# Optimization experiments

Hardware: AMD Instinct MI355X
Metric: run time of the kernel (lower is better)

Reference implementation:

```python
import jax, jax.numpy as jnp
import numpy as np

D = 384
H = 6
DK = D // H
EPS = 1e-5


def _layernorm(x, g, b):
    mu = jnp.mean(x, axis=-1, keepdims=True)
    var = jnp.var(x, axis=-1, keepdims=True)
    return (x - mu) * jax.lax.rsqrt(var + EPS) * g + b


def setup_inputs() -> dict:
    key = jax.random.key(0)
    ks = jax.random.split(key, 12)
    B, N = 8, 2048
    s = lambda fan_in: 1.0 / np.sqrt(fan_in)
    return {
        "points": jax.random.normal(ks[0], (B, 3 + D, N), dtype=jnp.float32),
        "ln1_g": jnp.ones((D,), jnp.float32),
        "ln1_b": jnp.zeros((D,), jnp.float32),
        "w_qkv": jax.random.uniform(ks[1], (3 * D, D), jnp.float32, -s(D), s(D)),
        "w_o": jax.random.uniform(ks[2], (D, D), jnp.float32, -s(D), s(D)),
        "b_o": jnp.zeros((D,), jnp.float32),
        "ln2_g": jnp.ones((D,), jnp.float32),
        "ln2_b": jnp.zeros((D,), jnp.float32),
        "w1": jax.random.uniform(ks[3], (2 * D, D), jnp.float32, -s(D), s(D)),
        "b1": jnp.zeros((2 * D,), jnp.float32),
        "w2": jax.random.uniform(ks[4], (D, 2 * D), jnp.float32, -s(2 * D), s(2 * D)),
        "b2": jnp.zeros((D,), jnp.float32),
    }


def reference(points, ln1_g, ln1_b, w_qkv, w_o, b_o, ln2_g, ln2_b, w1, b1, w2, b2):
    coords = points[:, :3, :]                       # [B, 3, N]
    feats = jnp.transpose(points[:, 3:, :], (0, 2, 1))  # [B, N, D]
    B, N, _ = feats.shape

    # pre-norm + fused QKV projection (no bias)
    h = _layernorm(feats, ln1_g, ln1_b)
    qkv = jnp.einsum('bnd,ed->bne', h, w_qkv)       # [B, N, 3D]
    q, k, v = jnp.split(qkv, 3, axis=-1)

    split_heads = lambda t: jnp.transpose(t.reshape(B, N, H, DK), (0, 2, 1, 3))
    q, k, v = split_heads(q), split_heads(k), split_heads(v)  # [B, H, N, DK]

    scale = DK ** -0.5
    scores = jnp.einsum('bhid,bhjd->bhij', q, k) * scale      # [B, H, N, N]
    attn = jax.nn.softmax(scores, axis=-1)
    ctx = jnp.einsum('bhij,bhjd->bhid', attn, v)              # [B, H, N, DK]
    ctx = jnp.transpose(ctx, (0, 2, 1, 3)).reshape(B, N, D)
    attn_out = jnp.einsum('bnd,ed->bne', ctx, w_o) + b_o

    x = feats + attn_out
    # FFN with exact (erf) GELU, hidden = 2*D
    h2 = _layernorm(x, ln2_g, ln2_b)
    ff = jnp.einsum('bnd,ed->bne', h2, w1) + b1
    ff = jax.nn.gelu(ff, approximate=False)
    ff = jnp.einsum('bne,de->bnd', ff, w2) + b2
    x = x + ff

    return jnp.concatenate([coords, jnp.transpose(x, (0, 2, 1))], axis=1)
```

## Files before the change

kernel.cpp:

```cpp
#include <hip/hip_runtime.h>
#include <cstdint>


typedef __bf16 bf16;
typedef __bf16 bf16x8 __attribute__((ext_vector_type(8)));
typedef __bf16 bf16x4 __attribute__((ext_vector_type(4)));
typedef float floatx4 __attribute__((ext_vector_type(4)));
typedef uint32_t __attribute__((address_space(1))) gu32;
typedef uint32_t __attribute__((address_space(3))) lu32;

#define NN 2048
#define DD 384
#define HH 6
#define DK 64
#define BB 8
#define MM (BB * NN)
#define D3 (3 * DD)
#define D2 (2 * DD)
#define CH (3 + DD)
#define LP 72


__global__ void cast_w_kernel(const float* __restrict__ in, bf16* __restrict__ out, int n) {
    int i = blockIdx.x * 256 + threadIdx.x;
    if (i < n) out[i] = (bf16)in[i];
}

__global__ void coords_kernel(const float* __restrict__ pts, float* __restrict__ out) {
    int i = blockIdx.x * 256 + threadIdx.x;
    int b = i / (3 * NN), r = i % (3 * NN);
    out[(size_t)b * CH * NN + r] = pts[(size_t)b * CH * NN + r];
}

__global__ void transpose_kernel(const float* __restrict__ pts, float* __restrict__ feats) {
    __shared__ float T[32][33];
    int n0 = blockIdx.x * 32, d0 = blockIdx.y * 32, b = blockIdx.z;
    int tx = threadIdx.x, ty = threadIdx.y;
    const float* src = pts + (size_t)b * CH * NN;
#pragma unroll
    for (int i = 0; i < 4; ++i)
        T[ty + i * 8][tx] = src[(size_t)(3 + d0 + ty + i * 8) * NN + n0 + tx];
    __syncthreads();
    float* dst = feats + (size_t)b * NN * DD;
#pragma unroll
    for (int i = 0; i < 4; ++i)
        dst[(size_t)(n0 + ty + i * 8) * DD + d0 + tx] = T[tx][ty + i * 8];
}

__global__ __launch_bounds__(256) void ln_kernel(const float* __restrict__ x,
                                                 const float* __restrict__ g,
                                                 const float* __restrict__ bta,
                                                 bf16* __restrict__ out) {
    int wave = threadIdx.x >> 6, lane = threadIdx.x & 63;
    int row = blockIdx.x * 4 + wave;
    const float* xr = x + (size_t)row * DD;
    float v[6], s = 0.f, sq = 0.f;
#pragma unroll
    for (int i = 0; i < 6; ++i) { v[i] = xr[lane + i * 64]; s += v[i]; sq += v[i] * v[i]; }
#pragma unroll
    for (int o = 1; o < 64; o <<= 1) { s += __shfl_xor(s, o); sq += __shfl_xor(sq, o); }
    float mu = s * (1.f / DD);
    float var = sq * (1.f / DD) - mu * mu;
    float rs = rsqrtf(var + 1e-5f);
    bf16* orow = out + (size_t)row * DD;
#pragma unroll
    for (int i = 0; i < 6; ++i) {
        int d = lane + i * 64;
        orow[d] = (bf16)((v[i] - mu) * rs * g[d] + bta[d]);
    }
}

template <int NC, int K, int MODE>
__global__ __launch_bounds__(256, 2)
void gemm_bt(const bf16* __restrict__ A, const bf16* __restrict__ W,
             const float* __restrict__ bias, const float* __restrict__ res,
             bf16* __restrict__ obf, float* __restrict__ of32, bf16* __restrict__ vt) {
    __shared__ bf16 As[128 * 32];
    __shared__ bf16 Ws[128 * 32];
    const int t = threadIdx.x;
    const int wave = t >> 6, lane = t & 63;
    const int m0 = blockIdx.x * 128, n0 = blockIdx.y * 128;
    const int wm = (wave >> 1) * 64, wn = (wave & 1) * 64;
    const int lr = lane & 15, quad = lane >> 4;
    const int sr = t >> 2, sc = (t & 3) * 8;

    floatx4 acc[4][4];
#pragma unroll
    for (int mi = 0; mi < 4; ++mi)
#pragma unroll
        for (int ni = 0; ni < 4; ++ni) {
            floatx4 z = {0.f, 0.f, 0.f, 0.f};
            acc[mi][ni] = z;
        }

    for (int k0 = 0; k0 < K; k0 += 32) {
        __syncthreads();
#pragma unroll
        for (int i = 0; i < 2; ++i) {
            const int r = i * 64 + sr;
            __builtin_amdgcn_global_load_lds(
                (const gu32*)&A[(size_t)(m0 + r) * K + k0 + sc],
                (lu32*)&As[r * 32 + sc], 16, 0, 0);
            __builtin_amdgcn_global_load_lds(
                (const gu32*)&W[(size_t)(n0 + r) * K + k0 + sc],
                (lu32*)&Ws[r * 32 + sc], 16, 0, 0);
        }
        __syncthreads();
        bf16x8 af[4], bfr[4];
#pragma unroll
        for (int mi = 0; mi < 4; ++mi)
            af[mi] = *(const bf16x8*)&As[(wm + mi * 16 + lr) * 32 + quad * 8];
#pragma unroll
        for (int ni = 0; ni < 4; ++ni)
            bfr[ni] = *(const bf16x8*)&Ws[(wn + ni * 16 + lr) * 32 + quad * 8];
#pragma unroll
        for (int mi = 0; mi < 4; ++mi)
#pragma unroll
            for (int ni = 0; ni < 4; ++ni)
                acc[mi][ni] = __builtin_amdgcn_mfma_f32_16x16x32_bf16(af[mi], bfr[ni], acc[mi][ni], 0, 0, 0);
    }

#pragma unroll
    for (int mi = 0; mi < 4; ++mi) {
#pragma unroll
        for (int ni = 0; ni < 4; ++ni) {
            const int r0 = m0 + wm + mi * 16 + quad * 4;
            const int c = n0 + wn + ni * 16 + lr;
            floatx4 v = acc[mi][ni];
            if constexpr (MODE == 0) {
                const int cb = n0 + wn + ni * 16;
                if (cb >= 2 * DD) {
                    const int hh = (c - 2 * DD) >> 6, dk = (c - 2 * DD) & 63;
                    const int b = r0 >> 11, n = r0 & (NN - 1);
                    bf16x4 pk;
#pragma unroll
                    for (int r = 0; r < 4; ++r) pk[r] = (bf16)v[r];
                    *(bf16x4*)&vt[((size_t)(b * HH + hh) * DK + dk) * NN + n] = pk;
                } else {
#pragma unroll
                    for (int r = 0; r < 4; ++r) obf[(size_t)(r0 + r) * NC + c] = (bf16)v[r];
                }
            } else if constexpr (MODE == 1) {
#pragma unroll
                for (int r = 0; r < 4; ++r)
                    of32[(size_t)(r0 + r) * NC + c] = v[r] + bias[c] + res[(size_t)(r0 + r) * NC + c];
            } else if constexpr (MODE == 2) {
#pragma unroll
                for (int r = 0; r < 4; ++r) {
                    float u = v[r] + bias[c];
                    obf[(size_t)(r0 + r) * NC + c] = (bf16)(0.5f * u * (1.f + erff(u * 0.70710678118f)));
                }
            } else {
                const int b = r0 >> 11, n = r0 & (NN - 1);
                float o4[4];
#pragma unroll
                for (int r = 0; r < 4; ++r)
                    o4[r] = v[r] + bias[c] + res[(size_t)(r0 + r) * DD + c];
                float4 val = make_float4(o4[0], o4[1], o4[2], o4[3]);
                *(float4*)&of32[((size_t)b * CH + 3 + c) * NN + n] = val;
            }
        }
    }
}

__global__ __launch_bounds__(256, 4)
void attn_kernel(const bf16* __restrict__ qkv, const bf16* __restrict__ vt,
                 bf16* __restrict__ ctx) {
    __shared__ bf16 Ks[64 * LP];
    __shared__ bf16 Vs[64 * LP];
    __shared__ bf16 Ps[4][32 * LP];
    const int t = threadIdx.x, wave = t >> 6, lane = t & 63;
    const int lr = lane & 15, quad = lane >> 4;
    const int bh = blockIdx.y, b = bh / HH, h = bh % HH;
    const int q0 = blockIdx.x * 128;
    const bf16* qbase = qkv + (size_t)b * NN * D3 + h * DK;
    const bf16* kbase = qbase + DD;
    const bf16* vbase = vt + (size_t)bh * DK * NN;

    bf16x8 aq[2][2];
#pragma unroll
    for (int mi = 0; mi < 2; ++mi)
#pragma unroll
        for (int ks = 0; ks < 2; ++ks)
            aq[mi][ks] = *(const bf16x8*)&qbase[(size_t)(q0 + wave * 32 + mi * 16 + lr) * D3 +
                                                ks * 32 + quad * 8];

    floatx4 o[2][4];
    float lrun[2][4];
#pragma unroll
    for (int mi = 0; mi < 2; ++mi) {
        floatx4 z = {0.f, 0.f, 0.f, 0.f};
#pragma unroll
        for (int nd = 0; nd < 4; ++nd) o[mi][nd] = z;
#pragma unroll
        for (int r = 0; r < 4; ++r) lrun[mi][r] = 0.f;
    }

    const float SC = 0.18033688011112042f;

    for (int j0 = 0; j0 < NN; j0 += 64) {
        __syncthreads();
        {
            const int rr = t >> 3, cc = (t & 7) * 8;
#pragma unroll
            for (int i = 0; i < 2; ++i) {
                const int j = i * 32 + rr;
                *(bf16x8*)&Ks[j * LP + cc] =
                    *(const bf16x8*)&kbase[(size_t)(j0 + j) * D3 + cc];
                *(bf16x8*)&Vs[j * LP + cc] =
                    *(const bf16x8*)&vbase[(size_t)j * NN + j0 + cc];
            }
        }
        __syncthreads();

        floatx4 s[2][4];
#pragma unroll
        for (int mi = 0; mi < 2; ++mi)
#pragma unroll
            for (int ni = 0; ni < 4; ++ni) {
                floatx4 z = {0.f, 0.f, 0.f, 0.f};
                s[mi][ni] = z;
            }
#pragma unroll
        for (int ks = 0; ks < 2; ++ks)
#pragma unroll
            for (int ni = 0; ni < 4; ++ni) {
                bf16x8 bk = *(const bf16x8*)&Ks[(ni * 16 + lr) * LP + ks * 32 + quad * 8];
#pragma unroll
                for (int mi = 0; mi < 2; ++mi)
                    s[mi][ni] = __builtin_amdgcn_mfma_f32_16x16x32_bf16(aq[mi][ks], bk, s[mi][ni], 0, 0, 0);
            }

#pragma unroll
        for (int mi = 0; mi < 2; ++mi) {
#pragma unroll
            for (int ni = 0; ni < 4; ++ni)
#pragma unroll
                for (int r = 0; r < 4; ++r) {
                    float p = exp2f(s[mi][ni][r] * SC);
                    s[mi][ni][r] = p;
                    lrun[mi][r] += p;
                }
#pragma unroll
            for (int ni = 0; ni < 4; ++ni)
#pragma unroll
                for (int r = 0; r < 4; ++r)
                    Ps[wave][(mi * 16 + quad * 4 + r) * LP + ni * 16 + lr] = (bf16)s[mi][ni][r];
        }

#pragma unroll
        for (int ks = 0; ks < 2; ++ks) {
            bf16x8 ap[2];
#pragma unroll
            for (int mi = 0; mi < 2; ++mi)
                ap[mi] = *(const bf16x8*)&Ps[wave][(mi * 16 + lr) * LP + ks * 32 + quad * 8];
#pragma unroll
            for (int nd = 0; nd < 4; ++nd) {
                bf16x8 bv = *(const bf16x8*)&Vs[(nd * 16 + lr) * LP + ks * 32 + quad * 8];
#pragma unroll
                for (int mi = 0; mi < 2; ++mi)
                    o[mi][nd] = __builtin_amdgcn_mfma_f32_16x16x32_bf16(ap[mi], bv, o[mi][nd], 0, 0, 0);
            }
        }
    }

#pragma unroll
    for (int off = 1; off < 16; off <<= 1)
#pragma unroll
        for (int mi = 0; mi < 2; ++mi)
#pragma unroll
            for (int r = 0; r < 4; ++r)
                lrun[mi][r] += __shfl_xor(lrun[mi][r], off);

#pragma unroll
    for (int mi = 0; mi < 2; ++mi)
#pragma unroll
        for (int r = 0; r < 4; ++r) {
            const int n = q0 + wave * 32 + mi * 16 + quad * 4 + r;
            const float inv = 1.0f / lrun[mi][r];
#pragma unroll
            for (int nd = 0; nd < 4; ++nd) {
                const int d = h * DK + nd * 16 + lr;
                ctx[(size_t)(b * NN + n) * DD + d] = (bf16)(o[mi][nd][r] * inv);
            }
        }
}


extern "C" void kernel_launch(void* const* d_in, const int* in_sizes, int n_in,
                              void* d_out, int out_size, void* d_ws, size_t ws_size,
                              hipStream_t stream) {
    const float* points = (const float*)d_in[0];
    const float* ln1_g = (const float*)d_in[1];
    const float* ln1_b = (const float*)d_in[2];
    const float* w_qkv = (const float*)d_in[3];
    const float* w_o   = (const float*)d_in[4];
    const float* b_o   = (const float*)d_in[5];
    const float* ln2_g = (const float*)d_in[6];
    const float* ln2_b = (const float*)d_in[7];
    const float* w1    = (const float*)d_in[8];
    const float* b1    = (const float*)d_in[9];
    const float* w2    = (const float*)d_in[10];
    const float* b2    = (const float*)d_in[11];
    float* out = (float*)d_out;

    char* ws = (char*)d_ws;
    size_t off = 0;
    auto alloc = [&](size_t bytes) -> void* {
        void* p = ws + off;
        off += (bytes + 255) & ~(size_t)255;
        return p;
    };
    float* feats = (float*)alloc((size_t)MM * DD * 4);
    float* xbuf  = (float*)alloc((size_t)MM * DD * 4);
    bf16* h1     = (bf16*)alloc((size_t)MM * DD * 2);
    bf16* h2     = (bf16*)alloc((size_t)MM * DD * 2);
    bf16* qkvb   = (bf16*)alloc((size_t)MM * D3 * 2);
    bf16* vtb    = (bf16*)alloc((size_t)BB * HH * DK * NN * 2);
    bf16* ctx    = (bf16*)alloc((size_t)MM * DD * 2);
    bf16* ffh    = (bf16*)alloc((size_t)MM * D2 * 2);
    bf16* wqkv_bf = (bf16*)alloc((size_t)D3 * DD * 2);
    bf16* wo_bf   = (bf16*)alloc((size_t)DD * DD * 2);
    bf16* w1_bf   = (bf16*)alloc((size_t)D2 * DD * 2);
    bf16* w2_bf   = (bf16*)alloc((size_t)DD * D2 * 2);

    cast_w_kernel<<<(D3 * DD + 255) / 256, 256, 0, stream>>>(w_qkv, wqkv_bf, D3 * DD);
    cast_w_kernel<<<(DD * DD + 255) / 256, 256, 0, stream>>>(w_o, wo_bf, DD * DD);
    cast_w_kernel<<<(D2 * DD + 255) / 256, 256, 0, stream>>>(w1, w1_bf, D2 * DD);
    cast_w_kernel<<<(DD * D2 + 255) / 256, 256, 0, stream>>>(w2, w2_bf, DD * D2);
    coords_kernel<<<(BB * 3 * NN) / 256, 256, 0, stream>>>(points, out);
    transpose_kernel<<<dim3(NN / 32, DD / 32, BB), dim3(32, 8), 0, stream>>>(points, feats);
    ln_kernel<<<MM / 4, 256, 0, stream>>>(feats, ln1_g, ln1_b, h1);
    gemm_bt<D3, DD, 0><<<dim3(MM / 128, D3 / 128), 256, 0, stream>>>(
        h1, wqkv_bf, nullptr, nullptr, qkvb, nullptr, vtb);
    attn_kernel<<<dim3(NN / 128, BB * HH), 256, 0, stream>>>(qkvb, vtb, ctx);
    gemm_bt<DD, DD, 1><<<dim3(MM / 128, DD / 128), 256, 0, stream>>>(
        ctx, wo_bf, b_o, feats, nullptr, xbuf, nullptr);
    ln_kernel<<<MM / 4, 256, 0, stream>>>(xbuf, ln2_g, ln2_b, h2);
    gemm_bt<D2, DD, 2><<<dim3(MM / 128, D2 / 128), 256, 0, stream>>>(
        h2, w1_bf, b1, nullptr, ffh, nullptr, nullptr);
    gemm_bt<DD, D2, 3><<<dim3(MM / 128, DD / 128), 256, 0, stream>>>(
        ffh, w2_bf, b2, xbuf, nullptr, out, nullptr);
}
```

Measured before the change: 321.4 us.

## Fold softmax scale into Q projection, transpose score MFMA, row-sum via MFMA

Pre-multiplies Q by the softmax scale (log2e/sqrt(dk)) in the QKV GEMM epilogue, so the attention loop computes exp2 directly. Swaps the MFMA operands for QK^T so each lane holds four consecutive key columns, letting P be stored to LDS as packed bf16x4 writes instead of scalar stores. The row-sum is now an extra MFMA against a ones vector on the bf16 P fragments, replacing per-element adds and the final shuffle reduction. This trades a few extra MFMAs per tile for fewer VALU ops and stores, and the denominator now sums bf16-rounded P, which matches the numerator.

```diff
diff --git a/kernel.cpp b/kernel.cpp
--- a/kernel.cpp
+++ b/kernel.cpp
@@ -19,6 +19,8 @@
 #define D2 (2 * DD)
 #define CH (3 + DD)
 #define LP 72
+
+#define QSCALE 0.18033688011112042f
 
 
 __global__ void cast_w_kernel(const float* __restrict__ in, bf16* __restrict__ out, int n) {
@@ -137,8 +139,9 @@
                     for (int r = 0; r < 4; ++r) pk[r] = (bf16)v[r];
                     *(bf16x4*)&vt[((size_t)(b * HH + hh) * DK + dk) * NN + n] = pk;
                 } else {
-#pragma unroll
-                    for (int r = 0; r < 4; ++r) obf[(size_t)(r0 + r) * NC + c] = (bf16)v[r];
+                    const float sc_q = (cb < DD) ? QSCALE : 1.0f;
+#pragma unroll
+                    for (int r = 0; r < 4; ++r) obf[(size_t)(r0 + r) * NC + c] = (bf16)(v[r] * sc_q);
                 }
             } else if constexpr (MODE == 1) {
 #pragma unroll
@@ -185,18 +188,18 @@
             aq[mi][ks] = *(const bf16x8*)&qbase[(size_t)(q0 + wave * 32 + mi * 16 + lr) * D3 +
                                                 ks * 32 + quad * 8];
 
-    floatx4 o[2][4];
-    float lrun[2][4];
+    bf16x8 ones;
+#pragma unroll
+    for (int i = 0; i < 8; ++i) ones[i] = (bf16)1.0f;
+
+    floatx4 o[2][4], ol[2];
 #pragma unroll
     for (int mi = 0; mi < 2; ++mi) {
         floatx4 z = {0.f, 0.f, 0.f, 0.f};
+        ol[mi] = z;
 #pragma unroll
         for (int nd = 0; nd < 4; ++nd) o[mi][nd] = z;
-#pragma unroll
-        for (int r = 0; r < 4; ++r) lrun[mi][r] = 0.f;
-    }
-
-    const float SC = 0.18033688011112042f;
+    }
 
     for (int j0 = 0; j0 < NN; j0 += 64) {
         __syncthreads();
@@ -217,36 +220,29 @@
 #pragma unroll
         for (int mi = 0; mi < 2; ++mi)
 #pragma unroll
-            for (int ni = 0; ni < 4; ++ni) {
+            for (int nj = 0; nj < 4; ++nj) {
                 floatx4 z = {0.f, 0.f, 0.f, 0.f};
-                s[mi][ni] = z;
+                s[mi][nj] = z;
             }
 #pragma unroll
         for (int ks = 0; ks < 2; ++ks)
 #pragma unroll
-            for (int ni = 0; ni < 4; ++ni) {
-                bf16x8 bk = *(const bf16x8*)&Ks[(ni * 16 + lr) * LP + ks * 32 + quad * 8];
+            for (int nj = 0; nj < 4; ++nj) {
+                bf16x8 bk = *(const bf16x8*)&Ks[(nj * 16 + lr) * LP + ks * 32 + quad * 8];
 #pragma unroll
                 for (int mi = 0; mi < 2; ++mi)
-                    s[mi][ni] = __builtin_amdgcn_mfma_f32_16x16x32_bf16(aq[mi][ks], bk, s[mi][ni], 0, 0, 0);
-            }
-
-#pragma unroll
-        for (int mi = 0; mi < 2; ++mi) {
-#pragma unroll
-            for (int ni = 0; ni < 4; ++ni)
-#pragma unroll
-                for (int r = 0; r < 4; ++r) {
-                    float p = exp2f(s[mi][ni][r] * SC);
-                    s[mi][ni][r] = p;
-                    lrun[mi][r] += p;
-                }
-#pragma unroll
-            for (int ni = 0; ni < 4; ++ni)
-#pragma unroll
-                for (int r = 0; r < 4; ++r)
-                    Ps[wave][(mi * 16 + quad * 4 + r) * LP + ni * 16 + lr] = (bf16)s[mi][ni][r];
-        }
+                    s[mi][nj] = __builtin_amdgcn_mfma_f32_16x16x32_bf16(bk, aq[mi][ks], s[mi][nj], 0, 0, 0);
+            }
+
+#pragma unroll
+        for (int mi = 0; mi < 2; ++mi)
+#pragma unroll
+            for (int nj = 0; nj < 4; ++nj) {
+                bf16x4 pk;
+#pragma unroll
+                for (int r = 0; r < 4; ++r) pk[r] = (bf16)exp2f(s[mi][nj][r]);
+                *(bf16x4*)&Ps[wave][(mi * 16 + lr) * LP + nj * 16 + quad * 4] = pk;
+            }
 
 #pragma unroll
         for (int ks = 0; ks < 2; ++ks) {
@@ -261,23 +257,18 @@
                 for (int mi = 0; mi < 2; ++mi)
                     o[mi][nd] = __builtin_amdgcn_mfma_f32_16x16x32_bf16(ap[mi], bv, o[mi][nd], 0, 0, 0);
             }
-        }
-    }
-
-#pragma unroll
-    for (int off = 1; off < 16; off <<= 1)
-#pragma unroll
-        for (int mi = 0; mi < 2; ++mi)
-#pragma unroll
-            for (int r = 0; r < 4; ++r)
-                lrun[mi][r] += __shfl_xor(lrun[mi][r], off);
+#pragma unroll
+            for (int mi = 0; mi < 2; ++mi)
+                ol[mi] = __builtin_amdgcn_mfma_f32_16x16x32_bf16(ap[mi], ones, ol[mi], 0, 0, 0);
+        }
+    }
 
 #pragma unroll
     for (int mi = 0; mi < 2; ++mi)
 #pragma unroll
         for (int r = 0; r < 4; ++r) {
             const int n = q0 + wave * 32 + mi * 16 + quad * 4 + r;
-            const float inv = 1.0f / lrun[mi][r];
+            const float inv = 1.0f / ol[mi][r];
 #pragma unroll
             for (int nd = 0; nd < 4; ++nd) {
                 const int d = h * DK + nd * 16 + lr;
```

Measured after the change: 308.5 us. 4.0% less time.
